# Kernel tuning notes

Measured on AMD Instinct MI355X. Metric: run time of the kernel, lower is better.

## Reference

```python
import jax, jax.numpy as jnp
import numpy as np

B, R, F, H, DIM = 256, 64, 2048, 512, 512

def setup_inputs() -> dict:
    key = jax.random.key(0)
    ks = jax.random.split(key, 8)
    s = lambda n: 1.0 / np.sqrt(n)
    return {
        "features": jax.random.normal(ks[0], (B, R, F), jnp.float32),
        "prev": jax.random.normal(ks[1], (B, H), jnp.float32),
        "W_w": jax.random.normal(ks[2], (F, DIM), jnp.float32) * s(F),
        "W_b": jnp.zeros((DIM,), jnp.float32),
        "W2_w": jax.random.normal(ks[3], (H, DIM), jnp.float32) * s(H),
        "W2_b": jnp.zeros((DIM,), jnp.float32),
        "W3_w": jax.random.normal(ks[4], (DIM, 1), jnp.float32) * s(DIM),
        "W3_b": jnp.zeros((1,), jnp.float32),
    }

def reference(features, prev, W_w, W_b, W2_w, W2_b, W3_w, W3_b):
    # prev: [B,H] -> [B,1,DIM]
    p = (prev @ W2_w + W2_b)[:, None, :]
    # features: [B,R,F] -> [B,R,DIM]
    c = jnp.einsum('brf,fd->brd', features, W_w) + W_b
    c = jnp.tanh(c + p)
    score = jnp.einsum('brd,do->bro', c, W3_w) + W3_b  # [B,R,1]
    aw = jax.nn.softmax(score, axis=1)
    q = jnp.sum(aw * features, axis=1)  # [B,F]
    return q
```

## Files before the change

kernel.cpp:

```cpp
#include <hip/hip_runtime.h>
#include <hip/hip_bf16.h>


#define B_ 256
#define R_ 64
#define F_ 2048
#define H_ 512
#define DIM_ 512

typedef short bf16x8 __attribute__((ext_vector_type(8)));
typedef float f32x4 __attribute__((ext_vector_type(4)));

__device__ __forceinline__ ushort f2bf(float x) {
  __hip_bfloat16 h = __float2bfloat16(x);
  return __builtin_bit_cast(ushort, h);
}

__device__ __forceinline__ uint4 pack8(float4 x, float4 y) {
  uint4 r;
  r.x = (uint)f2bf(x.x) | ((uint)f2bf(x.y) << 16);
  r.y = (uint)f2bf(x.z) | ((uint)f2bf(x.w) << 16);
  r.z = (uint)f2bf(y.x) | ((uint)f2bf(y.y) << 16);
  r.w = (uint)f2bf(y.z) | ((uint)f2bf(y.w) << 16);
  return r;
}

__device__ __forceinline__ void gld16(const float* g, float* l) {
  __builtin_amdgcn_global_load_lds(
      (const __attribute__((address_space(1))) unsigned int*)(g),
      (__attribute__((address_space(3))) unsigned int*)(l),
      16, 0, 0);
}

__global__ __launch_bounds__(256) void setup_k(const float* __restrict__ Ww,
                                               ushort* __restrict__ wpack,
                                               const float* __restrict__ prev,
                                               const float* __restrict__ W2w,
                                               const float* __restrict__ W2b,
                                               const float* __restrict__ Wb,
                                               float* __restrict__ pprime) {
  __shared__ float lprev[8][H_];
  if (blockIdx.x < 4096) {
    int idx = blockIdx.x * 256 + threadIdx.x;
    float v = Ww[idx];
    int k = idx >> 9;
    int d = idx & 511;
    int kt = k >> 5, kr = k & 31;
    int g = kr >> 3, i = kr & 7;
    int ctg = d >> 4, c = d & 15;
    size_t dst = ((size_t)((kt * 32 + ctg) * 64 + g * 16 + c)) * 8 + (size_t)i;
    wpack[dst] = f2bf(v);
    return;
  }
  int pb = blockIdx.x - 4096;
  int bg = pb >> 3;
  int d0 = (pb & 7) * 64;
  int t = threadIdx.x;
  const float4* src = reinterpret_cast<const float4*>(prev + (size_t)bg * 8 * H_);
  float4* dst = reinterpret_cast<float4*>(&lprev[0][0]);
  for (int i = t; i < 8 * H_ / 4; i += 256) dst[i] = src[i];
  __syncthreads();
  int d = d0 + (t & 63);
  int bq = t >> 6;
  float a0 = 0.f, a1 = 0.f;
  #pragma unroll 8
  for (int h = 0; h < H_; ++h) {
    float wv = W2w[h * DIM_ + d];
    a0 += lprev[bq][h] * wv;
    a1 += lprev[bq + 4][h] * wv;
  }
  float bias = W2b[d] + Wb[d];
  pprime[(size_t)(bg * 8 + bq) * DIM_ + d] = a0 + bias;
  pprime[(size_t)(bg * 8 + bq + 4) * DIM_ + d] = a1 + bias;
}

__device__ __forceinline__ float fast_tanh(float x) {
  float e = __expf(2.f * x);
  return 1.f - 2.f / (e + 1.f);
}

__global__ __launch_bounds__(512, 4) void score_k(const float* __restrict__ feat,
                                                  const ushort* __restrict__ wpack,
                                                  const float* __restrict__ pprime,
                                                  const float* __restrict__ W3,
                                                  float* __restrict__ sp) {
  int slice = blockIdx.x >> 8;
  int b = blockIdx.x & 255;
  int t = threadIdx.x;
  int wid = t >> 6;
  int l = t & 63;
  int l15 = l & 15, g = l >> 4;
  const float* featB = feat + (size_t)b * R_ * F_;

  __shared__ float raw[3][4096];
  __shared__ uint4 frg[2][512];
  __shared__ float lds_part[8][R_];

  f32x4 acc[4][2];
  #pragma unroll
  for (int rt = 0; rt < 4; ++rt)
    #pragma unroll
    for (int ct = 0; ct < 2; ++ct)
      acc[rt][ct] = (f32x4){0.f, 0.f, 0.f, 0.f};

  int srow = wid * 4 + g;
  int sch = l15 ^ (srow & 15);
  const float* sg0 = featB + (size_t)srow * F_ + sch * 4;
  const float* sg1 = featB + (size_t)(srow + 32) * F_ + sch * 4;

  int crow = t >> 3, cj2 = (t & 7) * 2;
  int rm = crow & 15;
  int cw = (t & 7) * 64 + (crow ^ cj2);

  const ushort* wp = wpack + (size_t)(slice * 16 + wid * 2) * 512 + (size_t)l * 8;

#define STAGE(buf, kt) do {                                        \
    gld16(sg0 + (size_t)(kt) * 64, &raw[buf][wid * 256]);          \
    gld16(sg1 + (size_t)(kt) * 64, &raw[buf][2048 + wid * 256]);   \
  } while (0)

#define LOADB(dst, kt) do {                                        \
    const ushort* wpk_ = wp + (size_t)(kt) * 32768;                \
    dst[0][0] = *reinterpret_cast<const uint4*>(wpk_);             \
    dst[0][1] = *reinterpret_cast<const uint4*>(wpk_ + 512);       \
    dst[1][0] = *reinterpret_cast<const uint4*>(wpk_ + 16384);     \
    dst[1][1] = *reinterpret_cast<const uint4*>(wpk_ + 16384 + 512); \
  } while (0)

#define CVT(nb, fb) do {                                           \
    const float* rb_ = &raw[nb][crow * 64];                        \
    float4 x_ = *reinterpret_cast<const float4*>(rb_ + ((cj2 + 0) ^ rm) * 4); \
    float4 y_ = *reinterpret_cast<const float4*>(rb_ + ((cj2 + 1) ^ rm) * 4); \
    frg[fb][cw] = pack8(x_, y_);                                   \
  } while (0)

#define MFMA_STEP(fb, BSET) do {                                   \
    _Pragma("unroll")                                              \
    for (int s_ = 0; s_ < 2; ++s_) {                               \
      bf16x8 af_[4];                                               \
      int kc_ = s_ * 4 + g;                                        \
      _Pragma("unroll")                                            \
      for (int rt_ = 0; rt_ < 4; ++rt_)                            \
        af_[rt_] = __builtin_bit_cast(bf16x8,                      \
            frg[fb][kc_ * 64 + ((rt_ * 16 + l15) ^ ((kc_ * 2) & 15))]); \
      _Pragma("unroll")                                            \
      for (int ct_ = 0; ct_ < 2; ++ct_) {                          \
        bf16x8 bv_ = __builtin_bit_cast(bf16x8, BSET[s_][ct_]);    \
        _Pragma("unroll")                                          \
        for (int rt_ = 0; rt_ < 4; ++rt_)                          \
          acc[rt_][ct_] = __builtin_amdgcn_mfma_f32_16x16x32_bf16( \
              af_[rt_], bv_, acc[rt_][ct_], 0, 0, 0);              \
      }                                                            \
    }                                                              \
  } while (0)

#define BARRIER_VM(N) do {                                         \
    asm volatile("s_waitcnt vmcnt(" #N ") lgkmcnt(0)" ::: "memory"); \
    __builtin_amdgcn_s_barrier();                                  \
    asm volatile("" ::: "memory");                                 \
  } while (0)

  uint4 bA[2][2], bB[2][2];
  STAGE(0, 0);
  STAGE(1, 1);
  LOADB(bA, 0);
  asm volatile("s_waitcnt vmcnt(6)" ::: "memory");
  __builtin_amdgcn_s_barrier();
  asm volatile("" ::: "memory");
  STAGE(2, 2);
  CVT(0, 0);

  int st_b = 0, cv_b = 1;
  for (int e = 0; e < 28; e += 2) {
    LOADB(bB, e + 1);
    BARRIER_VM(10);
    STAGE(st_b, e + 3);
    CVT(cv_b, 1);
    __builtin_amdgcn_s_setprio(1);
    MFMA_STEP(0, bA);
    __builtin_amdgcn_s_setprio(0);
    st_b = (st_b == 2) ? 0 : st_b + 1;
    cv_b = (cv_b == 2) ? 0 : cv_b + 1;
    LOADB(bA, e + 2);
    BARRIER_VM(10);
    STAGE(st_b, e + 4);
    CVT(cv_b, 0);
    __builtin_amdgcn_s_setprio(1);
    MFMA_STEP(1, bB);
    __builtin_amdgcn_s_setprio(0);
    st_b = (st_b == 2) ? 0 : st_b + 1;
    cv_b = (cv_b == 2) ? 0 : cv_b + 1;
  }
  LOADB(bB, 29);
  BARRIER_VM(10);
  STAGE(1, 31);
  CVT(2, 1);
  __builtin_amdgcn_s_setprio(1);
  MFMA_STEP(0, bA);
  __builtin_amdgcn_s_setprio(0);
  LOADB(bA, 30);
  BARRIER_VM(10);
  CVT(0, 0);
  __builtin_amdgcn_s_setprio(1);
  MFMA_STEP(1, bB);
  __builtin_amdgcn_s_setprio(0);
  LOADB(bB, 31);
  BARRIER_VM(8);
  CVT(1, 1);
  __builtin_amdgcn_s_setprio(1);
  MFMA_STEP(0, bA);
  __builtin_amdgcn_s_setprio(0);
  BARRIER_VM(0);
  __builtin_amdgcn_s_setprio(1);
  MFMA_STEP(1, bB);
  __builtin_amdgcn_s_setprio(0);

#undef STAGE
#undef LOADB
#undef CVT
#undef MFMA_STEP
#undef BARRIER_VM

  float pp[2], w3v[2];
  #pragma unroll
  for (int ct = 0; ct < 2; ++ct) {
    int col = slice * 256 + wid * 32 + ct * 16 + l15;
    pp[ct] = pprime[b * DIM_ + col];
    w3v[ct] = W3[col];
  }
  #pragma unroll
  for (int rt = 0; rt < 4; ++rt) {
    #pragma unroll
    for (int j = 0; j < 4; ++j) {
      float v = fast_tanh(acc[rt][0][j] + pp[0]) * w3v[0]
              + fast_tanh(acc[rt][1][j] + pp[1]) * w3v[1];
      v += __shfl_xor(v, 1);
      v += __shfl_xor(v, 2);
      v += __shfl_xor(v, 4);
      v += __shfl_xor(v, 8);
      if (l15 == 0) lds_part[wid][rt * 16 + g * 4 + j] = v;
    }
  }
  __syncthreads();

  if (t < R_) {
    float s = 0.f;
    #pragma unroll
    for (int w = 0; w < 8; ++w) s += lds_part[w][t];
    sp[((size_t)b * 2 + slice) * R_ + t] = s;
  }
}

__global__ __launch_bounds__(256) void wsum_k(const float* __restrict__ feat,
                                              const float* __restrict__ sp,
                                              float* __restrict__ out) {
  int b = blockIdx.x >> 2;
  int f0 = (blockIdx.x & 3) * 512;
  int t = threadIdx.x;
  __shared__ float lds_aw[R_];

  if (t < R_) {
    float s = sp[((size_t)b * 2 + 0) * R_ + t] + sp[((size_t)b * 2 + 1) * R_ + t];
    float m = s;
    #pragma unroll
    for (int off = 32; off >= 1; off >>= 1) m = fmaxf(m, __shfl_xor(m, off));
    float e = __expf(s - m);
    float su = e;
    #pragma unroll
    for (int off = 32; off >= 1; off >>= 1) su += __shfl_xor(su, off);
    lds_aw[t] = e / su;
  }
  __syncthreads();

  const float* fp = feat + (size_t)b * R_ * F_ + f0 + t * 2;
  float qx = 0.f, qy = 0.f;
  #pragma unroll 8
  for (int r = 0; r < R_; ++r) {
    float a = lds_aw[r];
    float2 v = *reinterpret_cast<const float2*>(fp + (size_t)r * F_);
    qx += a * v.x;
    qy += a * v.y;
  }
  *reinterpret_cast<float2*>(out + (size_t)b * F_ + f0 + t * 2) = (float2){qx, qy};
}

extern "C" void kernel_launch(void* const* d_in, const int* in_sizes, int n_in,
                              void* d_out, int out_size, void* d_ws, size_t ws_size,
                              hipStream_t stream) {
  const float* feat = (const float*)d_in[0];
  const float* prev = (const float*)d_in[1];
  const float* Ww   = (const float*)d_in[2];
  const float* Wb   = (const float*)d_in[3];
  const float* W2w  = (const float*)d_in[4];
  const float* W2b  = (const float*)d_in[5];
  const float* W3w  = (const float*)d_in[6];
  float* out = (float*)d_out;

  ushort* wpack  = (ushort*)d_ws;
  float*  pprime = (float*)((char*)d_ws + (size_t)F_ * DIM_ * 2);
  float*  sp     = (float*)((char*)d_ws + (size_t)F_ * DIM_ * 2
                                        + (size_t)B_ * DIM_ * 4);

  setup_k<<<4096 + 256, 256, 0, stream>>>(Ww, wpack, prev, W2w, W2b, Wb, pprime);
  score_k<<<B_ * 2, 512, 0, stream>>>(feat, wpack, pprime, W3w, sp);
  wsum_k<<<B_ * 4, 256, 0, stream>>>(feat, sp, out);
}
```

Baseline: 98.37 us.

## Replace LDS-direct feature staging with register prefetch and wider K super-steps

Feature tiles are now loaded with float4 global loads straight into registers (8 rows per wave, 256 K-columns per super-step) instead of async global_load_lds into a triple-buffered raw fp32 LDS area. The bf16 conversion then writes a larger double-buffered fragment buffer that covers four MFMA sub-steps. This removes the fp32 LDS round trip and cuts the number of conversion phases and barriers per K element. In exchange it uses more VGPRs for the prefetched rows, which may hurt occupancy, and it relies on retuned vmcnt waits.

```diff
diff --git a/kernel.cpp b/kernel.cpp
--- a/kernel.cpp
+++ b/kernel.cpp
@@ -16,20 +16,11 @@
   return __builtin_bit_cast(ushort, h);
 }
 
-__device__ __forceinline__ uint4 pack8(float4 x, float4 y) {
-  uint4 r;
+__device__ __forceinline__ uint2 pack4(float4 x) {
+  uint2 r;
   r.x = (uint)f2bf(x.x) | ((uint)f2bf(x.y) << 16);
   r.y = (uint)f2bf(x.z) | ((uint)f2bf(x.w) << 16);
-  r.z = (uint)f2bf(y.x) | ((uint)f2bf(y.y) << 16);
-  r.w = (uint)f2bf(y.z) | ((uint)f2bf(y.w) << 16);
   return r;
-}
-
-__device__ __forceinline__ void gld16(const float* g, float* l) {
-  __builtin_amdgcn_global_load_lds(
-      (const __attribute__((address_space(1))) unsigned int*)(g),
-      (__attribute__((address_space(3))) unsigned int*)(l),
-      16, 0, 0);
 }
 
 __global__ __launch_bounds__(256) void setup_k(const float* __restrict__ Ww,
@@ -92,8 +83,7 @@
   int l15 = l & 15, g = l >> 4;
   const float* featB = feat + (size_t)b * R_ * F_;
 
-  __shared__ float raw[3][4096];
-  __shared__ uint4 frg[2][512];
+  __shared__ uint4 frg[2][2048];
   __shared__ float lds_part[8][R_];
 
   f32x4 acc[4][2];
@@ -103,20 +93,19 @@
     for (int ct = 0; ct < 2; ++ct)
       acc[rt][ct] = (f32x4){0.f, 0.f, 0.f, 0.f};
 
-  int srow = wid * 4 + g;
-  int sch = l15 ^ (srow & 15);
-  const float* sg0 = featB + (size_t)srow * F_ + sch * 4;
-  const float* sg1 = featB + (size_t)(srow + 32) * F_ + sch * 4;
-
-  int crow = t >> 3, cj2 = (t & 7) * 2;
-  int rm = crow & 15;
-  int cw = (t & 7) * 64 + (crow ^ cj2);
+  const float* abase = featB + (size_t)(wid * 8) * F_ + (size_t)(l * 4);
+  float4 rA[8];
+
+  int kcl = l >> 1;
+  int whalf = l & 1;
 
   const ushort* wp = wpack + (size_t)(slice * 16 + wid * 2) * 512 + (size_t)l * 8;
 
-#define STAGE(buf, kt) do {                                        \
-    gld16(sg0 + (size_t)(kt) * 64, &raw[buf][wid * 256]);          \
-    gld16(sg1 + (size_t)(kt) * 64, &raw[buf][2048 + wid * 256]);   \
+#define LOADA(S) do {                                              \
+    const float* ap_ = abase + (size_t)(S) * 256;                  \
+    _Pragma("unroll")                                              \
+    for (int j_ = 0; j_ < 8; ++j_)                                 \
+      rA[j_] = *reinterpret_cast<const float4*>(ap_ + (size_t)j_ * F_); \
   } while (0)
 
 #define LOADB(dst, kt) do {                                        \
@@ -127,22 +116,25 @@
     dst[1][1] = *reinterpret_cast<const uint4*>(wpk_ + 16384 + 512); \
   } while (0)
 
-#define CVT(nb, fb) do {                                           \
-    const float* rb_ = &raw[nb][crow * 64];                        \
-    float4 x_ = *reinterpret_cast<const float4*>(rb_ + ((cj2 + 0) ^ rm) * 4); \
-    float4 y_ = *reinterpret_cast<const float4*>(rb_ + ((cj2 + 1) ^ rm) * 4); \
-    frg[fb][cw] = pack8(x_, y_);                                   \
-  } while (0)
-
-#define MFMA_STEP(fb, BSET) do {                                   \
+#define CVT(fb) do {                                               \
+    _Pragma("unroll")                                              \
+    for (int j_ = 0; j_ < 8; ++j_) {                               \
+      int row_ = wid * 8 + j_;                                     \
+      int idx_ = kcl * 64 + (row_ ^ (kcl & 15));                   \
+      uint2 pk_ = pack4(rA[j_]);                                   \
+      *(reinterpret_cast<uint2*>(&frg[fb][idx_]) + whalf) = pk_;   \
+    }                                                              \
+  } while (0)
+
+#define MFMA_SUB(fb, tt, BSET) do {                                \
     _Pragma("unroll")                                              \
     for (int s_ = 0; s_ < 2; ++s_) {                               \
+      int kcg_ = (tt) * 8 + s_ * 4 + g;                            \
       bf16x8 af_[4];                                               \
-      int kc_ = s_ * 4 + g;                                        \
       _Pragma("unroll")                                            \
       for (int rt_ = 0; rt_ < 4; ++rt_)                            \
         af_[rt_] = __builtin_bit_cast(bf16x8,                      \
-            frg[fb][kc_ * 64 + ((rt_ * 16 + l15) ^ ((kc_ * 2) & 15))]); \
+            frg[fb][kcg_ * 64 + ((rt_ * 16 + l15) ^ (kcg_ & 15))]); \
       _Pragma("unroll")                                            \
       for (int ct_ = 0; ct_ < 2; ++ct_) {                          \
         bf16x8 bv_ = __builtin_bit_cast(bf16x8, BSET[s_][ct_]);    \
@@ -161,64 +153,60 @@
   } while (0)
 
   uint4 bA[2][2], bB[2][2];
-  STAGE(0, 0);
-  STAGE(1, 1);
+  LOADA(0);
   LOADB(bA, 0);
-  asm volatile("s_waitcnt vmcnt(6)" ::: "memory");
-  __builtin_amdgcn_s_barrier();
-  asm volatile("" ::: "memory");
-  STAGE(2, 2);
-  CVT(0, 0);
-
-  int st_b = 0, cv_b = 1;
-  for (int e = 0; e < 28; e += 2) {
-    LOADB(bB, e + 1);
-    BARRIER_VM(10);
-    STAGE(st_b, e + 3);
-    CVT(cv_b, 1);
-    __builtin_amdgcn_s_setprio(1);
-    MFMA_STEP(0, bA);
-    __builtin_amdgcn_s_setprio(0);
-    st_b = (st_b == 2) ? 0 : st_b + 1;
-    cv_b = (cv_b == 2) ? 0 : cv_b + 1;
-    LOADB(bA, e + 2);
-    BARRIER_VM(10);
-    STAGE(st_b, e + 4);
-    CVT(cv_b, 0);
-    __builtin_amdgcn_s_setprio(1);
-    MFMA_STEP(1, bB);
-    __builtin_amdgcn_s_setprio(0);
-    st_b = (st_b == 2) ? 0 : st_b + 1;
-    cv_b = (cv_b == 2) ? 0 : cv_b + 1;
+  asm volatile("s_waitcnt vmcnt(4)" ::: "memory");
+  CVT(0);
+
+  for (int S = 0; S < 7; ++S) {
+    int fb = S & 1;
+    LOADB(bB, S * 4 + 1);
+    LOADA(S + 1);
+    BARRIER_VM(12);
+    __builtin_amdgcn_s_setprio(1);
+    MFMA_SUB(fb, 0, bA);
+    __builtin_amdgcn_s_setprio(0);
+    LOADB(bA, S * 4 + 2);
+    BARRIER_VM(12);
+    __builtin_amdgcn_s_setprio(1);
+    MFMA_SUB(fb, 1, bB);
+    __builtin_amdgcn_s_setprio(0);
+    LOADB(bB, S * 4 + 3);
+    BARRIER_VM(4);
+    __builtin_amdgcn_s_setprio(1);
+    MFMA_SUB(fb, 2, bA);
+    __builtin_amdgcn_s_setprio(0);
+    LOADB(bA, S * 4 + 4);
+    BARRIER_VM(4);
+    CVT(fb ^ 1);
+    __builtin_amdgcn_s_setprio(1);
+    MFMA_SUB(fb, 3, bB);
+    __builtin_amdgcn_s_setprio(0);
   }
   LOADB(bB, 29);
-  BARRIER_VM(10);
-  STAGE(1, 31);
-  CVT(2, 1);
-  __builtin_amdgcn_s_setprio(1);
-  MFMA_STEP(0, bA);
+  BARRIER_VM(4);
+  __builtin_amdgcn_s_setprio(1);
+  MFMA_SUB(1, 0, bA);
   __builtin_amdgcn_s_setprio(0);
   LOADB(bA, 30);
-  BARRIER_VM(10);
-  CVT(0, 0);
-  __builtin_amdgcn_s_setprio(1);
-  MFMA_STEP(1, bB);
+  BARRIER_VM(4);
+  __builtin_amdgcn_s_setprio(1);
+  MFMA_SUB(1, 1, bB);
   __builtin_amdgcn_s_setprio(0);
   LOADB(bB, 31);
-  BARRIER_VM(8);
-  CVT(1, 1);
-  __builtin_amdgcn_s_setprio(1);
-  MFMA_STEP(0, bA);
+  BARRIER_VM(4);
+  __builtin_amdgcn_s_setprio(1);
+  MFMA_SUB(1, 2, bA);
   __builtin_amdgcn_s_setprio(0);
   BARRIER_VM(0);
   __builtin_amdgcn_s_setprio(1);
-  MFMA_STEP(1, bB);
-  __builtin_amdgcn_s_setprio(0);
-
-#undef STAGE
+  MFMA_SUB(1, 3, bB);
+  __builtin_amdgcn_s_setprio(0);
+
+#undef LOADA
 #undef LOADB
 #undef CVT
-#undef MFMA_STEP
+#undef MFMA_SUB
 #undef BARRIER_VM
 
   float pp[2], w3v[2];
```

Measured after the change: 175.3 us. 78.2% more time.

## Fuse softmax weighted-sum into score kernel via last-block atomic counter

Applied to the files above, without the earlier changes.

Removes the separate wsum kernel. Each of the two slice blocks per batch increments a per-batch atomic counter, and the block that finishes last reads both partial scores, computes the softmax and the weighted feature sum over all F columns with float4 loads. This saves a kernel launch and may hit cached feature data, but the weighted sum now runs on only 256 blocks, each covering the full F range. It also adds a memset and fence/atomic overhead.

```diff
diff --git a/kernel.cpp b/kernel.cpp
--- a/kernel.cpp
+++ b/kernel.cpp
@@ -83,7 +83,9 @@
                                                   const ushort* __restrict__ wpack,
                                                   const float* __restrict__ pprime,
                                                   const float* __restrict__ W3,
-                                                  float* __restrict__ sp) {
+                                                  float* __restrict__ sp,
+                                                  int* __restrict__ cnt,
+                                                  float* __restrict__ out) {
   int slice = blockIdx.x >> 8;
   int b = blockIdx.x & 255;
   int t = threadIdx.x;
@@ -95,6 +97,8 @@
   __shared__ float raw[3][4096];
   __shared__ uint4 frg[2][512];
   __shared__ float lds_part[8][R_];
+  __shared__ float lds_aw[R_];
+  __shared__ int is_last;
 
   f32x4 acc[4][2];
   #pragma unroll
@@ -249,18 +253,23 @@
     for (int w = 0; w < 8; ++w) s += lds_part[w][t];
     sp[((size_t)b * 2 + slice) * R_ + t] = s;
   }
-}
-
-__global__ __launch_bounds__(256) void wsum_k(const float* __restrict__ feat,
-                                              const float* __restrict__ sp,
-                                              float* __restrict__ out) {
-  int b = blockIdx.x >> 2;
-  int f0 = (blockIdx.x & 3) * 512;
-  int t = threadIdx.x;
-  __shared__ float lds_aw[R_];
+  __threadfence();
+  __syncthreads();
+
+  if (t == 0) {
+    int old = __hip_atomic_fetch_add(&cnt[b], 1, __ATOMIC_ACQ_REL,
+                                     __HIP_MEMORY_SCOPE_AGENT);
+    is_last = (old == 1);
+  }
+  __syncthreads();
+  if (!is_last) return;
 
   if (t < R_) {
-    float s = sp[((size_t)b * 2 + 0) * R_ + t] + sp[((size_t)b * 2 + 1) * R_ + t];
+    float s0 = __hip_atomic_load(&sp[((size_t)b * 2 + 0) * R_ + t],
+                                 __ATOMIC_RELAXED, __HIP_MEMORY_SCOPE_AGENT);
+    float s1 = __hip_atomic_load(&sp[((size_t)b * 2 + 1) * R_ + t],
+                                 __ATOMIC_RELAXED, __HIP_MEMORY_SCOPE_AGENT);
+    float s = s0 + s1;
     float m = s;
     #pragma unroll
     for (int off = 32; off >= 1; off >>= 1) m = fmaxf(m, __shfl_xor(m, off));
@@ -272,16 +281,18 @@
   }
   __syncthreads();
 
-  const float* fp = feat + (size_t)b * R_ * F_ + f0 + t * 2;
-  float qx = 0.f, qy = 0.f;
-  #pragma unroll 8
-  for (int r = 0; r < R_; ++r) {
-    float a = lds_aw[r];
-    float2 v = *reinterpret_cast<const float2*>(fp + (size_t)r * F_);
-    qx += a * v.x;
-    qy += a * v.y;
-  }
-  *reinterpret_cast<float2*>(out + (size_t)b * F_ + f0 + t * 2) = (float2){qx, qy};
+  {
+    int f0 = t * 4;
+    float4 qa = (float4){0.f, 0.f, 0.f, 0.f};
+    const float* fp = featB + f0;
+    #pragma unroll 8
+    for (int r = 0; r < R_; ++r) {
+      float a = lds_aw[r];
+      float4 v = *reinterpret_cast<const float4*>(fp + (size_t)r * F_);
+      qa.x += a * v.x; qa.y += a * v.y; qa.z += a * v.z; qa.w += a * v.w;
+    }
+    *reinterpret_cast<float4*>(out + (size_t)b * F_ + f0) = qa;
+  }
 }
 
 extern "C" void kernel_launch(void* const* d_in, const int* in_sizes, int n_in,
@@ -296,12 +307,16 @@
   const float* W3w  = (const float*)d_in[6];
   float* out = (float*)d_out;
 
-  ushort* wpack  = (ushort*)d_ws;
-  float*  pprime = (float*)((char*)d_ws + (size_t)F_ * DIM_ * 2);
-  float*  sp     = (float*)((char*)d_ws + (size_t)F_ * DIM_ * 2
-                                        + (size_t)B_ * DIM_ * 4);
-
+  char* ws = (char*)d_ws;
+  ushort* wpack  = (ushort*)ws;
+  float*  pprime = (float*)(ws + (size_t)F_ * DIM_ * 2);
+  float*  sp     = (float*)(ws + (size_t)F_ * DIM_ * 2
+                               + (size_t)B_ * DIM_ * 4);
+  int*    cnt    = (int*)(ws + (size_t)F_ * DIM_ * 2
+                             + (size_t)B_ * DIM_ * 4
+                             + (size_t)B_ * 2 * R_ * 4);
+
+  hipMemsetAsync(cnt, 0, B_ * sizeof(int), stream);
   setup_k<<<4096 + 256, 256, 0, stream>>>(Ww, wpack, prev, W2w, W2b, Wb, pprime);
-  score_k<<<B_ * 2, 512, 0, stream>>>(feat, wpack, pprime, W3w, sp);
-  wsum_k<<<B_ * 4, 256, 0, stream>>>(feat, sp, out);
-}
+  score_k<<<B_ * 2, 512, 0, stream>>>(feat, wpack, pprime, W3w, sp, cnt, out);
+}
```

Result: slower. 161.2 us (+63.9%).
